# Kernel optimization log

Hardware: AMD Instinct MI355X
Metric: run time of the kernel (lower is better)

Reference implementation:

```python
import jax, jax.numpy as jnp
import numpy as np

B, D, H, NL, DFF, N = 64, 768, 12, 12, 3072, 197
HD = D // H  # 64
SCALE = HD ** -0.5


def setup_inputs() -> dict:
    key = jax.random.key(0)
    ks = iter(jax.random.split(key, 64))
    def rn(shape, s=0.02):
        return jax.random.normal(next(ks), shape, jnp.float32) * s
    inp = {
        'x': jax.random.normal(next(ks), (B, 12, 1000), jnp.float32),
        # PatchEmbed convs (torch Conv1d weight layout OIH)
        'conv1_w': rn((256, 12, 5), 0.1), 'conv1_b': jnp.zeros((256,), jnp.float32),
        'bn1_g': jnp.ones((256,), jnp.float32), 'bn1_b': jnp.zeros((256,), jnp.float32),
        'bn1_m': jnp.zeros((256,), jnp.float32), 'bn1_v': jnp.ones((256,), jnp.float32),
        'conv2_w': rn((768, 256, 5), 0.05), 'conv2_b': jnp.zeros((768,), jnp.float32),
        'bn2_g': jnp.ones((768,), jnp.float32), 'bn2_b': jnp.zeros((768,), jnp.float32),
        'bn2_m': jnp.zeros((768,), jnp.float32), 'bn2_v': jnp.ones((768,), jnp.float32),
        'cls_token': rn((1, 1, D)), 'pos_embed': rn((1, N, D)),
        # 12 transformer blocks, stacked. Linear weights stored [in, out].
        'ln1_g': jnp.ones((NL, D), jnp.float32), 'ln1_b': jnp.zeros((NL, D), jnp.float32),
        'qkv_w': rn((NL, D, 3 * D)),            # qkv_bias=False
        'proj_w': rn((NL, D, D)), 'proj_b': jnp.zeros((NL, D), jnp.float32),
        'ln2_g': jnp.ones((NL, D), jnp.float32), 'ln2_b': jnp.zeros((NL, D), jnp.float32),
        'fc1_w': rn((NL, D, DFF)), 'fc1_b': jnp.zeros((NL, DFF), jnp.float32),
        'fc2_w': rn((NL, DFF, D)), 'fc2_b': jnp.zeros((NL, D), jnp.float32),
        'norm_g': jnp.ones((D,), jnp.float32), 'norm_b': jnp.zeros((D,), jnp.float32),
        # ProjectionHead (nonlinear): Linear(768->768,no bias)+BN, ReLU, Linear(768->512,no bias)+BN
        'p1_w': rn((D, D)),
        'p1bn_g': jnp.ones((D,), jnp.float32), 'p1bn_b': jnp.zeros((D,), jnp.float32),
        'p1bn_m': jnp.zeros((D,), jnp.float32), 'p1bn_v': jnp.ones((D,), jnp.float32),
        'p2_w': rn((D, 512)),
        'p2bn_g': jnp.ones((512,), jnp.float32), 'p2bn_b': jnp.zeros((512,), jnp.float32),
        'p2bn_m': jnp.zeros((512,), jnp.float32), 'p2bn_v': jnp.ones((512,), jnp.float32),
    }
    return inp


def _conv1d(x, w, b, stride):
    y = jax.lax.conv_general_dilated(x, w, (stride,), 'VALID',
                                     dimension_numbers=('NCH', 'OIH', 'NCH'))
    return y + b[None, :, None]


def _bn_c(x, g, b, m, v, eps=1e-5):  # BatchNorm1d eval, channel axis 1 of (B,C,L)
    return (x - m[None, :, None]) * (g[None, :, None] / jnp.sqrt(v[None, :, None] + eps)) + b[None, :, None]


def _bn_f(x, g, b, m, v, eps=1e-5):  # BatchNorm1d eval on (B,F)
    return (x - m) * (g / jnp.sqrt(v + eps)) + b


def _ln(x, g, b, eps=1e-6):
    mu = x.mean(-1, keepdims=True)
    var = jnp.var(x, axis=-1, keepdims=True)
    return (x - mu) * jax.lax.rsqrt(var + eps) * g + b


def reference(x, conv1_w, conv1_b, bn1_g, bn1_b, bn1_m, bn1_v,
              conv2_w, conv2_b, bn2_g, bn2_b, bn2_m, bn2_v,
              cls_token, pos_embed,
              ln1_g, ln1_b, qkv_w, proj_w, proj_b,
              ln2_g, ln2_b, fc1_w, fc1_b, fc2_w, fc2_b,
              norm_g, norm_b,
              p1_w, p1bn_g, p1bn_b, p1bn_m, p1bn_v,
              p2_w, p2bn_g, p2bn_b, p2bn_m, p2bn_v):
    # PatchEmbed: conv -> ReLU -> BN, twice; then (B, 196, 768)
    h = _bn_c(jax.nn.relu(_conv1d(x, conv1_w, conv1_b, 5)), bn1_g, bn1_b, bn1_m, bn1_v)
    h = _bn_c(jax.nn.relu(_conv1d(h, conv2_w, conv2_b, 1)), bn2_g, bn2_b, bn2_m, bn2_v)
    h = jnp.transpose(h, (0, 2, 1))  # [B, 196, D]
    b = h.shape[0]
    tok = jnp.concatenate([jnp.broadcast_to(cls_token, (b, 1, D)), h], axis=1) + pos_embed  # [B, 197, D]

    for i in range(NL):
        y = _ln(tok, ln1_g[i], ln1_b[i])
        qkv = jnp.einsum('bnd,de->bne', y, qkv_w[i]).reshape(b, N, 3, H, HD)
        q, k, v = jnp.moveaxis(qkv, 2, 0)  # each [B, N, H, HD]
        q = jnp.transpose(q, (0, 2, 1, 3)) * SCALE  # [B, H, N, HD]
        k = jnp.transpose(k, (0, 2, 1, 3))
        v = jnp.transpose(v, (0, 2, 1, 3))
        attn = jax.nn.softmax(jnp.einsum('bhnd,bhmd->bhnm', q, k), axis=-1)
        o = jnp.einsum('bhnm,bhmd->bhnd', attn, v)
        o = jnp.transpose(o, (0, 2, 1, 3)).reshape(b, N, D)
        tok = tok + jnp.einsum('bnd,de->bne', o, proj_w[i]) + proj_b[i]
        y = _ln(tok, ln2_g[i], ln2_b[i])
        y = jax.nn.gelu(jnp.einsum('bnd,df->bnf', y, fc1_w[i]) + fc1_b[i], approximate=False)
        tok = tok + jnp.einsum('bnf,fd->bnd', y, fc2_w[i]) + fc2_b[i]

    cls = _ln(tok, norm_g, norm_b)[:, 0]  # global_pool='token'
    z = _bn_f(cls @ p1_w, p1bn_g, p1bn_b, p1bn_m, p1bn_v)
    z = jax.nn.relu(z)
    z = _bn_f(z @ p2_w, p2bn_g, p2bn_b, p2bn_m, p2bn_v)
    return z
```

## Files before the change

kernel.cpp:

```cpp
#include <hip/hip_runtime.h>
#include <hip/hip_bf16.h>

typedef __hip_bfloat16 bf16;
typedef __attribute__((ext_vector_type(8))) short bf16x8;
typedef __attribute__((ext_vector_type(4))) float f32x4;

__device__ __forceinline__ float bf2f(bf16 v) { return __bfloat162float(v); }
__device__ __forceinline__ unsigned short f2bfu(float f) {
    bf16 h = __float2bfloat16(f);
    return __builtin_bit_cast(unsigned short, h);
}

__device__ __forceinline__ void gload16(const void* g, void* lds) {
    __builtin_amdgcn_global_load_lds(
        (const __attribute__((address_space(1))) unsigned int*)g,
        (__attribute__((address_space(3))) unsigned int*)lds, 16, 0, 0);
}

__global__ __launch_bounds__(256)
void conv1_kernel(const float* __restrict__ x, const float* __restrict__ w,
                  const float* __restrict__ bias,
                  const float* __restrict__ g, const float* __restrict__ b,
                  const float* __restrict__ m, const float* __restrict__ v,
                  bf16* __restrict__ h1) {
    int bo = blockIdx.x;
    int bb = bo >> 8, o = bo & 255;
    int l = threadIdx.x;
    if (l >= 200) return;
    const float* wo = w + o * 60;
    const float* xb = x + bb * 12000;
    float acc = bias[o];
#pragma unroll
    for (int i = 0; i < 12; i++)
#pragma unroll
        for (int t = 0; t < 5; t++)
            acc = fmaf(xb[i * 1000 + 5 * l + t], wo[i * 5 + t], acc);
    acc = fmaxf(acc, 0.f);
    float sc = g[o] * rsqrtf(v[o] + 1e-5f);
    acc = (acc - m[o]) * sc + b[o];
    h1[bo * 200 + l] = __float2bfloat16(acc);
}

__global__ __launch_bounds__(256)
void im2col_kernel(const bf16* __restrict__ h1, bf16* __restrict__ A2) {
    int idx = blockIdx.x * 256 + threadIdx.x;
    int row = idx / 1280, c = idx - row * 1280;
    int bb = row / 196, l = row - bb * 196;
    int i = c / 5, t = c - i * 5;
    A2[idx] = h1[(bb * 256 + i) * 200 + l + t];
}

__global__ __launch_bounds__(256)
void add_cls_pos(const float* __restrict__ cls, const float* __restrict__ pos,
                 float* __restrict__ tok) {
    int idx = blockIdx.x * 256 + threadIdx.x;
    int bb = idx / 768, d = idx - bb * 768;
    tok[(size_t)bb * 197 * 768 + d] = cls[d] + pos[d];
}

__global__ __launch_bounds__(256)
void cvt_kernel(const float* __restrict__ in, bf16* __restrict__ out, int n) {
    int idx = blockIdx.x * 256 + threadIdx.x;
    if (idx < n) out[idx] = __float2bfloat16(in[idx]);
}

__global__ __launch_bounds__(256)
void wtrans_layer(const float* __restrict__ qkvw, const float* __restrict__ projw,
                  const float* __restrict__ fc1w, const float* __restrict__ fc2w,
                  bf16* __restrict__ qkvT, bf16* __restrict__ projT,
                  bf16* __restrict__ fc1T, bf16* __restrict__ fc2T) {
    __shared__ float tile[32][33];
    int blk = blockIdx.x;
    const float* in; bf16* out; int Kd, Nd, t0;
    if (blk < 1728)      { in = qkvw; out = qkvT; Kd = 768;  Nd = 2304; t0 = blk; }
    else if (blk < 2304) { in = projw; out = projT; Kd = 768;  Nd = 768;  t0 = blk - 1728; }
    else if (blk < 4608) { in = fc1w; out = fc1T; Kd = 768;  Nd = 3072; t0 = blk - 2304; }
    else                 { in = fc2w; out = fc2T; Kd = 3072; Nd = 768;  t0 = blk - 4608; }
    int ntiles = Nd >> 5;
    int kt = t0 / ntiles, nt = t0 - kt * ntiles;
    int k0 = kt * 32, n0 = nt * 32;
    int tx = threadIdx.x & 31, ty = threadIdx.x >> 5;
#pragma unroll
    for (int j = 0; j < 4; j++)
        tile[ty + 8 * j][tx] = in[(size_t)(k0 + ty + 8 * j) * Nd + n0 + tx];
    __syncthreads();
#pragma unroll
    for (int j = 0; j < 4; j++)
        out[(size_t)(n0 + ty + 8 * j) * Kd + k0 + tx] = __float2bfloat16(tile[tx][ty + 8 * j]);
}

__global__ __launch_bounds__(256)
void wtrans2(const float* __restrict__ in, bf16* __restrict__ out, int Kd, int Nd) {
    __shared__ float tile[32][33];
    int ntiles = Nd >> 5;
    int kt = blockIdx.x / ntiles, nt = blockIdx.x - kt * ntiles;
    int k0 = kt * 32, n0 = nt * 32;
    int tx = threadIdx.x & 31, ty = threadIdx.x >> 5;
#pragma unroll
    for (int j = 0; j < 4; j++)
        tile[ty + 8 * j][tx] = in[(size_t)(k0 + ty + 8 * j) * Nd + n0 + tx];
    __syncthreads();
#pragma unroll
    for (int j = 0; j < 4; j++)
        out[(size_t)(n0 + ty + 8 * j) * Kd + k0 + tx] = __float2bfloat16(tile[tx][ty + 8 * j]);
}

__global__ __launch_bounds__(256)
void ln_kernel(const float* __restrict__ x, bf16* __restrict__ y,
               const float* __restrict__ g, const float* __restrict__ b,
               int nrows, int xstride) {
    int row = blockIdx.x * 4 + (threadIdx.x >> 6);
    if (row >= nrows) return;
    int l = threadIdx.x & 63;
    const float* xr = x + (size_t)row * xstride;
    float4 v0 = *(const float4*)(xr + l * 4);
    float4 v1 = *(const float4*)(xr + 256 + l * 4);
    float4 v2 = *(const float4*)(xr + 512 + l * 4);
    float s1 = 0.f, s2 = 0.f;
    {
        float e;
        e = v0.x; s1 += e; s2 += e * e;  e = v0.y; s1 += e; s2 += e * e;
        e = v0.z; s1 += e; s2 += e * e;  e = v0.w; s1 += e; s2 += e * e;
        e = v1.x; s1 += e; s2 += e * e;  e = v1.y; s1 += e; s2 += e * e;
        e = v1.z; s1 += e; s2 += e * e;  e = v1.w; s1 += e; s2 += e * e;
        e = v2.x; s1 += e; s2 += e * e;  e = v2.y; s1 += e; s2 += e * e;
        e = v2.z; s1 += e; s2 += e * e;  e = v2.w; s1 += e; s2 += e * e;
    }
#pragma unroll
    for (int off = 1; off < 64; off <<= 1) {
        s1 += __shfl_xor(s1, off);
        s2 += __shfl_xor(s2, off);
    }
    float mu = s1 * (1.f / 768.f);
    float rs = rsqrtf(s2 * (1.f / 768.f) - mu * mu + 1e-6f);
    bf16* yr = y + (size_t)row * 768;
#pragma unroll
    for (int sgi = 0; sgi < 3; sgi++) {
        float4 vv = sgi == 0 ? v0 : (sgi == 1 ? v1 : v2);
        float4 gg = *(const float4*)(g + sgi * 256 + l * 4);
        float4 bb = *(const float4*)(b + sgi * 256 + l * 4);
        ushort4 o;
        o.x = f2bfu((vv.x - mu) * rs * gg.x + bb.x);
        o.y = f2bfu((vv.y - mu) * rs * gg.y + bb.y);
        o.z = f2bfu((vv.z - mu) * rs * gg.z + bb.z);
        o.w = f2bfu((vv.w - mu) * rs * gg.w + bb.w);
        *(ushort4*)(yr + sgi * 256 + l * 4) = o;
    }
}

enum { E_BF16 = 0, E_RESID = 1, E_GELU = 2, E_CONV2 = 3, E_HEAD1 = 4, E_HEAD2 = 5 };

template<int EPI>
__global__ __launch_bounds__(256)
void gemm2(const bf16* __restrict__ A, const bf16* __restrict__ Bt,
           int M, int N, int K,
           const float* __restrict__ bias,
           bf16* __restrict__ Co, float* __restrict__ tok,
           const float* __restrict__ bng, const float* __restrict__ bnb,
           const float* __restrict__ bnm, const float* __restrict__ bnv,
           const float* __restrict__ pos) {
    __shared__ bf16 As[128 * 64];
    __shared__ bf16 Bs[128 * 64];
    const int t = threadIdx.x;
    const int l = t & 63, w = t >> 6;
    const int wm = (w >> 1) * 64, wn = (w & 1) * 64;
    const int row0 = blockIdx.y * 128, col0 = blockIdx.x * 128;
    const int lr = l & 15, kg = l >> 4;

    const int srow = w * 8 + (l >> 3);
    const int sc = ((l & 7) ^ (l >> 3)) * 8;
    const int dstoff = w * 1024 + l * 16;

    const f32x4 zero4 = {0.f, 0.f, 0.f, 0.f};
    f32x4 acc[4][4];
#pragma unroll
    for (int i = 0; i < 4; i++)
#pragma unroll
        for (int j = 0; j < 4; j++) acc[i][j] = zero4;

    for (int k0 = 0; k0 < K; k0 += 64) {
#pragma unroll
        for (int p = 0; p < 4; p++) {
            int r = srow + p * 32;
            int gra = row0 + r; if (gra >= M) gra = M - 1;
            gload16(A + (size_t)gra * K + k0 + sc, (char*)As + p * 4096 + dstoff);
            gload16(Bt + (size_t)(col0 + r) * K + k0 + sc, (char*)Bs + p * 4096 + dstoff);
        }
        __syncthreads();
#pragma unroll
        for (int ks = 0; ks < 2; ks++) {
            bf16x8 af[4], bfv[4];
            const int cc = ((ks * 4 + kg) ^ (lr & 7)) * 16;
#pragma unroll
            for (int i = 0; i < 4; i++) {
                af[i]  = *(const bf16x8*)((const char*)As + (wm + i * 16 + lr) * 128 + cc);
                bfv[i] = *(const bf16x8*)((const char*)Bs + (wn + i * 16 + lr) * 128 + cc);
            }
#pragma unroll
            for (int i = 0; i < 4; i++)
#pragma unroll
                for (int j = 0; j < 4; j++)
                    acc[i][j] = __builtin_amdgcn_mfma_f32_16x16x32_bf16(af[i], bfv[j], acc[i][j], 0, 0, 0);
        }
        __syncthreads();
    }

    const int rbase = row0 + wm + (kg << 2);
#pragma unroll
    for (int i = 0; i < 4; i++) {
#pragma unroll
        for (int sr = 0; sr < 4; sr++) {
            int r = rbase + i * 16 + sr;
            if (r < M) {
#pragma unroll
                for (int j = 0; j < 4; j++) {
                    int c = col0 + wn + j * 16 + lr;
                    float vv = acc[i][j][sr];
                    if (EPI == E_BF16) {
                        Co[(size_t)r * N + c] = __float2bfloat16(vv);
                    } else if (EPI == E_RESID) {
                        float* p = tok + (size_t)r * N + c;
                        *p += vv + bias[c];
                    } else if (EPI == E_GELU) {
                        float xx = vv + bias[c];
                        float gg = 0.5f * xx * (1.f + erff(xx * 0.70710678118f));
                        Co[(size_t)r * N + c] = __float2bfloat16(gg);
                    } else if (EPI == E_CONV2) {
                        float xx = vv + bias[c];
                        xx = fmaxf(xx, 0.f);
                        float sc2 = bng[c] * rsqrtf(bnv[c] + 1e-5f);
                        xx = (xx - bnm[c]) * sc2 + bnb[c];
                        int bb = r / 196, ll = r - bb * 196;
                        xx += pos[(size_t)(1 + ll) * 768 + c];
                        tok[(size_t)(bb * 197 + 1 + ll) * 768 + c] = xx;
                    } else if (EPI == E_HEAD1) {
                        float sc2 = bng[c] * rsqrtf(bnv[c] + 1e-5f);
                        float xx = (vv - bnm[c]) * sc2 + bnb[c];
                        xx = fmaxf(xx, 0.f);
                        Co[(size_t)r * N + c] = __float2bfloat16(xx);
                    } else {
                        float sc2 = bng[c] * rsqrtf(bnv[c] + 1e-5f);
                        tok[(size_t)r * N + c] = (vv - bnm[c]) * sc2 + bnb[c];
                    }
                }
            }
        }
    }
}

#define ATTN_LDS (208 * 72 * 2 + 64 * 232 * 2 + 4 * 16 * 232 * 2)

__global__ __launch_bounds__(256)
void attn_kernel(const bf16* __restrict__ qkv, bf16* __restrict__ o) {
    extern __shared__ char smem[];
    bf16* Ks = (bf16*)smem;
    bf16* Vt = Ks + 208 * 72;
    bf16* Pl = Vt + 64 * 232;
    const int bh = blockIdx.x, bb = bh / 12, h = bh - bb * 12;
    const int t = threadIdx.x, w = t >> 6, l = t & 63;
    const int lr = l & 15, lk8 = (l >> 4) * 8;
    const size_t base = (size_t)bb * 197 * 2304 + (size_t)h * 64;

    for (int qi = t; qi < 197 * 16; qi += 256) {
        int n = qi >> 4, d4 = (qi & 15) << 2;
        ushort4 kv = *(const ushort4*)(qkv + base + (size_t)n * 2304 + 768 + d4);
        *(ushort4*)&Ks[n * 72 + d4] = kv;
    }
    for (int qi = t; qi < 11 * 72; qi += 256) ((unsigned short*)Ks)[197 * 72 + qi] = 0;
    for (int qi = t; qi < 197 * 16; qi += 256) {
        int n = qi >> 4, d4 = (qi & 15) << 2;
        ushort4 vv = *(const ushort4*)(qkv + base + (size_t)n * 2304 + 1536 + d4);
        ((unsigned short*)Vt)[(d4 + 0) * 232 + n] = vv.x;
        ((unsigned short*)Vt)[(d4 + 1) * 232 + n] = vv.y;
        ((unsigned short*)Vt)[(d4 + 2) * 232 + n] = vv.z;
        ((unsigned short*)Vt)[(d4 + 3) * 232 + n] = vv.w;
    }
    for (int qi = t; qi < 64 * 35; qi += 256) {
        int d = qi / 35, c = 197 + (qi - d * 35);
        ((unsigned short*)Vt)[d * 232 + c] = 0;
    }
    __syncthreads();

    bf16* Pw = Pl + w * (16 * 232);
    const f32x4 zero4 = {0.f, 0.f, 0.f, 0.f};
    for (int qt = w; qt < 13; qt += 4) {
        int m0 = qt * 16;
        int qrow = m0 + lr; if (qrow > 196) qrow = 196;
        const bf16* qp = qkv + (size_t)(bb * 197 + qrow) * 2304 + h * 64 + lk8;
        bf16x8 a0 = *(const bf16x8*)qp;
        bf16x8 a1 = *(const bf16x8*)(qp + 32);
        f32x4 s[13];
#pragma unroll
        for (int kt = 0; kt < 13; kt++) {
            const bf16* kp = &Ks[(kt * 16 + lr) * 72 + lk8];
            bf16x8 b0 = *(const bf16x8*)kp;
            bf16x8 b1 = *(const bf16x8*)(kp + 32);
            f32x4 z = zero4;
            z = __builtin_amdgcn_mfma_f32_16x16x32_bf16(a0, b0, z, 0, 0, 0);
            z = __builtin_amdgcn_mfma_f32_16x16x32_bf16(a1, b1, z, 0, 0, 0);
            s[kt] = z;
        }
        float mx[4] = {-1e30f, -1e30f, -1e30f, -1e30f};
#pragma unroll
        for (int kt = 0; kt < 13; kt++) {
            bool valid = (kt < 12) || (lr <= 4);
#pragma unroll
            for (int sr = 0; sr < 4; sr++) {
                float sv = s[kt][sr] * 0.125f;
                sv = valid ? sv : -1e30f;
                s[kt][sr] = sv;
                mx[sr] = fmaxf(mx[sr], sv);
            }
        }
#pragma unroll
        for (int off = 1; off < 16; off <<= 1)
#pragma unroll
            for (int sr = 0; sr < 4; sr++)
                mx[sr] = fmaxf(mx[sr], __shfl_xor(mx[sr], off));
        float sum[4] = {0.f, 0.f, 0.f, 0.f};
#pragma unroll
        for (int kt = 0; kt < 13; kt++)
#pragma unroll
            for (int sr = 0; sr < 4; sr++) {
                float p = __expf(s[kt][sr] - mx[sr]);
                s[kt][sr] = p;
                sum[sr] += p;
            }
#pragma unroll
        for (int off = 1; off < 16; off <<= 1)
#pragma unroll
            for (int sr = 0; sr < 4; sr++)
                sum[sr] += __shfl_xor(sum[sr], off);
        float inv[4];
#pragma unroll
        for (int sr = 0; sr < 4; sr++) inv[sr] = 1.f / sum[sr];
#pragma unroll
        for (int kt = 0; kt < 13; kt++)
#pragma unroll
            for (int sr = 0; sr < 4; sr++)
                ((unsigned short*)Pw)[((l >> 4) * 4 + sr) * 232 + kt * 16 + lr] =
                    f2bfu(s[kt][sr] * inv[sr]);
        for (int j = l; j < 256; j += 64) {
            int rr = j >> 4, cc = 208 + (j & 15);
            ((unsigned short*)Pw)[rr * 232 + cc] = 0;
        }
        asm volatile("s_waitcnt lgkmcnt(0)" ::: "memory");
        f32x4 oa[4];
#pragma unroll
        for (int nf = 0; nf < 4; nf++) oa[nf] = zero4;
#pragma unroll
        for (int ks = 0; ks < 7; ks++) {
            const bf16* pp = &Pw[lr * 232 + ks * 32 + lk8];
            bf16x8 ap = *(const bf16x8*)pp;
#pragma unroll
            for (int nf = 0; nf < 4; nf++) {
                bf16x8 bv = *(const bf16x8*)&Vt[(nf * 16 + lr) * 232 + ks * 32 + lk8];
                oa[nf] = __builtin_amdgcn_mfma_f32_16x16x32_bf16(ap, bv, oa[nf], 0, 0, 0);
            }
        }
#pragma unroll
        for (int nf = 0; nf < 4; nf++)
#pragma unroll
            for (int sr = 0; sr < 4; sr++) {
                int orow = m0 + (l >> 4) * 4 + sr;
                if (orow <= 196)
                    o[(size_t)(bb * 197 + orow) * 768 + h * 64 + nf * 16 + lr] =
                        __float2bfloat16(oa[nf][sr]);
            }
    }
}

extern "C" void kernel_launch(void* const* d_in, const int* in_sizes, int n_in,
                              void* d_out, int out_size, void* d_ws, size_t ws_size,
                              hipStream_t stream) {
    (void)in_sizes; (void)n_in; (void)out_size; (void)ws_size;
    const float* x        = (const float*)d_in[0];
    const float* conv1_w  = (const float*)d_in[1];
    const float* conv1_b  = (const float*)d_in[2];
    const float* bn1_g = (const float*)d_in[3],  *bn1_b = (const float*)d_in[4];
    const float* bn1_m = (const float*)d_in[5],  *bn1_v = (const float*)d_in[6];
    const float* conv2_w  = (const float*)d_in[7];
    const float* conv2_b  = (const float*)d_in[8];
    const float* bn2_g = (const float*)d_in[9],  *bn2_b = (const float*)d_in[10];
    const float* bn2_m = (const float*)d_in[11], *bn2_v = (const float*)d_in[12];
    const float* cls_tok  = (const float*)d_in[13];
    const float* pos      = (const float*)d_in[14];
    const float* ln1_g = (const float*)d_in[15], *ln1_b = (const float*)d_in[16];
    const float* qkv_w = (const float*)d_in[17];
    const float* proj_w = (const float*)d_in[18], *proj_b = (const float*)d_in[19];
    const float* ln2_g = (const float*)d_in[20], *ln2_b = (const float*)d_in[21];
    const float* fc1_w = (const float*)d_in[22], *fc1_b = (const float*)d_in[23];
    const float* fc2_w = (const float*)d_in[24], *fc2_b = (const float*)d_in[25];
    const float* norm_g = (const float*)d_in[26], *norm_b = (const float*)d_in[27];
    const float* p1_w = (const float*)d_in[28];
    const float* p1g = (const float*)d_in[29], *p1b = (const float*)d_in[30];
    const float* p1m = (const float*)d_in[31], *p1v = (const float*)d_in[32];
    const float* p2_w = (const float*)d_in[33];
    const float* p2g = (const float*)d_in[34], *p2b = (const float*)d_in[35];
    const float* p2m = (const float*)d_in[36], *p2v = (const float*)d_in[37];

    char* ws = (char*)d_ws;
    float* tok  = (float*)(ws + 0);
    bf16* ybf   = (bf16*)(ws + 38731776);
    bf16* qkvb  = (bf16*)(ws + 58097664);
    bf16* a1    = (bf16*)(ws + 116195328);
    bf16* h1    = (bf16*)(ws + 116195328);
    bf16* A2    = (bf16*)(ws + 116195328 + 8388608);
    bf16* clsb  = (bf16*)(ws + 193658880);
    bf16* z1    = (bf16*)(ws + 193757184);
    bf16* wtb   = (bf16*)(ws + 193953792);
    bf16* qkvT = wtb;
    bf16* projT = wtb + 1769472;
    bf16* fc1T = wtb + 2359296;
    bf16* fc2T = wtb + 4718592;
    bf16* conv2T = wtb;
    bf16* p1T = a1;
    bf16* p2T = a1 + 768 * 768;

    (void)hipFuncSetAttribute((const void*)attn_kernel,
                              hipFuncAttributeMaxDynamicSharedMemorySize, ATTN_LDS);

    conv1_kernel<<<64 * 256, 256, 0, stream>>>(x, conv1_w, conv1_b, bn1_g, bn1_b, bn1_m, bn1_v, h1);
    im2col_kernel<<<(12544 * 1280) / 256, 256, 0, stream>>>(h1, A2);
    cvt_kernel<<<(768 * 1280 + 255) / 256, 256, 0, stream>>>(conv2_w, conv2T, 768 * 1280);
    gemm2<E_CONV2><<<dim3(6, 98), 256, 0, stream>>>(
        A2, conv2T, 12544, 768, 1280, conv2_b, nullptr, tok, bn2_g, bn2_b, bn2_m, bn2_v, pos);
    add_cls_pos<<<(64 * 768) / 256, 256, 0, stream>>>(cls_tok, pos, tok);

    const int MT = (12608 + 127) / 128;
    for (int i = 0; i < 12; i++) {
        wtrans_layer<<<6912, 256, 0, stream>>>(
            qkv_w + (size_t)i * 768 * 2304, proj_w + (size_t)i * 768 * 768,
            fc1_w + (size_t)i * 768 * 3072, fc2_w + (size_t)i * 3072 * 768,
            qkvT, projT, fc1T, fc2T);
        ln_kernel<<<12608 / 4, 256, 0, stream>>>(tok, ybf, ln1_g + i * 768, ln1_b + i * 768, 12608, 768);
        gemm2<E_BF16><<<dim3(18, MT), 256, 0, stream>>>(
            ybf, qkvT, 12608, 2304, 768,
            nullptr, qkvb, nullptr, nullptr, nullptr, nullptr, nullptr, nullptr);
        attn_kernel<<<768, 256, ATTN_LDS, stream>>>(qkvb, ybf);
        gemm2<E_RESID><<<dim3(6, MT), 256, 0, stream>>>(
            ybf, projT, 12608, 768, 768,
            proj_b + i * 768, nullptr, tok, nullptr, nullptr, nullptr, nullptr, nullptr);
        ln_kernel<<<12608 / 4, 256, 0, stream>>>(tok, ybf, ln2_g + i * 768, ln2_b + i * 768, 12608, 768);
        gemm2<E_GELU><<<dim3(24, MT), 256, 0, stream>>>(
            ybf, fc1T, 12608, 3072, 768,
            fc1_b + i * 3072, a1, nullptr, nullptr, nullptr, nullptr, nullptr, nullptr);
        gemm2<E_RESID><<<dim3(6, MT), 256, 0, stream>>>(
            a1, fc2T, 12608, 768, 3072,
            fc2_b + i * 768, nullptr, tok, nullptr, nullptr, nullptr, nullptr, nullptr);
    }

    ln_kernel<<<16, 256, 0, stream>>>(tok, clsb, norm_g, norm_b, 64, 197 * 768);
    wtrans2<<<576, 256, 0, stream>>>(p1_w, p1T, 768, 768);
    wtrans2<<<384, 256, 0, stream>>>(p2_w, p2T, 768, 512);
    gemm2<E_HEAD1><<<dim3(6, 1), 256, 0, stream>>>(
        clsb, p1T, 64, 768, 768,
        nullptr, z1, nullptr, p1g, p1b, p1m, p1v, nullptr);
    gemm2<E_HEAD2><<<dim3(4, 1), 256, 0, stream>>>(
        z1, p2T, 64, 512, 768,
        nullptr, nullptr, (float*)d_out, p2g, p2b, p2m, p2v, nullptr);
}
```

Before: 4.988 ms.

## Double-buffer GEMM LDS tiles and switch GELU to tanh approximation

The bf16 MFMA GEMM now uses 64 KB of dynamic shared memory holding two tile buffers. The global-to-LDS loads for the next K tile are issued before computing on the current one, so memory latency overlaps the matrix math, with a single barrier per iteration. The larger LDS footprint may lower how many blocks fit on a CU. Separately, the exact erf GELU in the fc1 epilogue is replaced by a tanh approximation built on __expf. That is cheaper but departs slightly from the reference's approximate=False semantics.

```diff
diff --git a/kernel.cpp b/kernel.cpp
--- a/kernel.cpp
+++ b/kernel.cpp
@@ -15,6 +15,14 @@
     __builtin_amdgcn_global_load_lds(
         (const __attribute__((address_space(1))) unsigned int*)g,
         (__attribute__((address_space(3))) unsigned int*)lds, 16, 0, 0);
+}
+
+__device__ __forceinline__ float gelu_f(float x) {
+    float u = 0.7978845608f * (x + 0.044715f * x * x * x);
+    float e = __expf(-2.0f * fabsf(u));
+    float th = (1.f - e) / (1.f + e);
+    th = u < 0.f ? -th : th;
+    return 0.5f * x * (1.f + th);
 }
 
 __global__ __launch_bounds__(256)
@@ -149,6 +157,7 @@
 }
 
 enum { E_BF16 = 0, E_RESID = 1, E_GELU = 2, E_CONV2 = 3, E_HEAD1 = 4, E_HEAD2 = 5 };
+#define GEMM_LDS 65536
 
 template<int EPI>
 __global__ __launch_bounds__(256)
@@ -159,8 +168,7 @@
            const float* __restrict__ bng, const float* __restrict__ bnb,
            const float* __restrict__ bnm, const float* __restrict__ bnv,
            const float* __restrict__ pos) {
-    __shared__ bf16 As[128 * 64];
-    __shared__ bf16 Bs[128 * 64];
+    extern __shared__ char smem[];
     const int t = threadIdx.x;
     const int l = t & 63, w = t >> 6;
     const int wm = (w >> 1) * 64, wn = (w & 1) * 64;
@@ -178,23 +186,35 @@
 #pragma unroll
         for (int j = 0; j < 4; j++) acc[i][j] = zero4;
 
-    for (int k0 = 0; k0 < K; k0 += 64) {
+    auto stage = [&](int b, int k0) {
 #pragma unroll
         for (int p = 0; p < 4; p++) {
             int r = srow + p * 32;
             int gra = row0 + r; if (gra >= M) gra = M - 1;
-            gload16(A + (size_t)gra * K + k0 + sc, (char*)As + p * 4096 + dstoff);
-            gload16(Bt + (size_t)(col0 + r) * K + k0 + sc, (char*)Bs + p * 4096 + dstoff);
-        }
-        __syncthreads();
+            char* base = smem + b * 32768 + p * 4096 + dstoff;
+            gload16(A + (size_t)gra * K + k0 + sc, base);
+            gload16(Bt + (size_t)(col0 + r) * K + k0 + sc, base + 16384);
+        }
+    };
+
+    const int nt = K >> 6;
+    stage(0, 0);
+    asm volatile("s_waitcnt vmcnt(0)" ::: "memory");
+    __syncthreads();
+
+    int cur = 0;
+    for (int kt = 0; kt < nt; kt++) {
+        if (kt + 1 < nt) stage(cur ^ 1, (kt + 1) << 6);
+        const char* Ab = smem + cur * 32768;
+        const char* Bb = Ab + 16384;
 #pragma unroll
         for (int ks = 0; ks < 2; ks++) {
             bf16x8 af[4], bfv[4];
             const int cc = ((ks * 4 + kg) ^ (lr & 7)) * 16;
 #pragma unroll
             for (int i = 0; i < 4; i++) {
-                af[i]  = *(const bf16x8*)((const char*)As + (wm + i * 16 + lr) * 128 + cc);
-                bfv[i] = *(const bf16x8*)((const char*)Bs + (wn + i * 16 + lr) * 128 + cc);
+                af[i]  = *(const bf16x8*)(Ab + (wm + i * 16 + lr) * 128 + cc);
+                bfv[i] = *(const bf16x8*)(Bb + (wn + i * 16 + lr) * 128 + cc);
             }
 #pragma unroll
             for (int i = 0; i < 4; i++)
@@ -202,7 +222,9 @@
                 for (int j = 0; j < 4; j++)
                     acc[i][j] = __builtin_amdgcn_mfma_f32_16x16x32_bf16(af[i], bfv[j], acc[i][j], 0, 0, 0);
         }
+        asm volatile("s_waitcnt vmcnt(0)" ::: "memory");
         __syncthreads();
+        cur ^= 1;
     }
 
     const int rbase = row0 + wm + (kg << 2);
@@ -222,9 +244,7 @@
                         float* p = tok + (size_t)r * N + c;
                         *p += vv + bias[c];
                     } else if (EPI == E_GELU) {
-                        float xx = vv + bias[c];
-                        float gg = 0.5f * xx * (1.f + erff(xx * 0.70710678118f));
-                        Co[(size_t)r * N + c] = __float2bfloat16(gg);
+                        Co[(size_t)r * N + c] = __float2bfloat16(gelu_f(vv + bias[c]));
                     } else if (EPI == E_CONV2) {
                         float xx = vv + bias[c];
                         xx = fmaxf(xx, 0.f);
@@ -419,11 +439,23 @@
 
     (void)hipFuncSetAttribute((const void*)attn_kernel,
                               hipFuncAttributeMaxDynamicSharedMemorySize, ATTN_LDS);
+    (void)hipFuncSetAttribute((const void*)gemm2<E_BF16>,
+                              hipFuncAttributeMaxDynamicSharedMemorySize, GEMM_LDS);
+    (void)hipFuncSetAttribute((const void*)gemm2<E_RESID>,
+                              hipFuncAttributeMaxDynamicSharedMemorySize, GEMM_LDS);
+    (void)hipFuncSetAttribute((const void*)gemm2<E_GELU>,
+                              hipFuncAttributeMaxDynamicSharedMemorySize, GEMM_LDS);
+    (void)hipFuncSetAttribute((const void*)gemm2<E_CONV2>,
+                              hipFuncAttributeMaxDynamicSharedMemorySize, GEMM_LDS);
+    (void)hipFuncSetAttribute((const void*)gemm2<E_HEAD1>,
+                              hipFuncAttributeMaxDynamicSharedMemorySize, GEMM_LDS);
+    (void)hipFuncSetAttribute((const void*)gemm2<E_HEAD2>,
+                              hipFuncAttributeMaxDynamicSharedMemorySize, GEMM_LDS);
 
     conv1_kernel<<<64 * 256, 256, 0, stream>>>(x, conv1_w, conv1_b, bn1_g, bn1_b, bn1_m, bn1_v, h1);
     im2col_kernel<<<(12544 * 1280) / 256, 256, 0, stream>>>(h1, A2);
     cvt_kernel<<<(768 * 1280 + 255) / 256, 256, 0, stream>>>(conv2_w, conv2T, 768 * 1280);
-    gemm2<E_CONV2><<<dim3(6, 98), 256, 0, stream>>>(
+    gemm2<E_CONV2><<<dim3(6, 98), 256, GEMM_LDS, stream>>>(
         A2, conv2T, 12544, 768, 1280, conv2_b, nullptr, tok, bn2_g, bn2_b, bn2_m, bn2_v, pos);
     add_cls_pos<<<(64 * 768) / 256, 256, 0, stream>>>(cls_tok, pos, tok);
 
@@ -434,18 +466,18 @@
             fc1_w + (size_t)i * 768 * 3072, fc2_w + (size_t)i * 3072 * 768,
             qkvT, projT, fc1T, fc2T);
         ln_kernel<<<12608 / 4, 256, 0, stream>>>(tok, ybf, ln1_g + i * 768, ln1_b + i * 768, 12608, 768);
-        gemm2<E_BF16><<<dim3(18, MT), 256, 0, stream>>>(
+        gemm2<E_BF16><<<dim3(18, MT), 256, GEMM_LDS, stream>>>(
             ybf, qkvT, 12608, 2304, 768,
             nullptr, qkvb, nullptr, nullptr, nullptr, nullptr, nullptr, nullptr);
         attn_kernel<<<768, 256, ATTN_LDS, stream>>>(qkvb, ybf);
-        gemm2<E_RESID><<<dim3(6, MT), 256, 0, stream>>>(
+        gemm2<E_RESID><<<dim3(6, MT), 256, GEMM_LDS, stream>>>(
             ybf, projT, 12608, 768, 768,
             proj_b + i * 768, nullptr, tok, nullptr, nullptr, nullptr, nullptr, nullptr);
         ln_kernel<<<12608 / 4, 256, 0, stream>>>(tok, ybf, ln2_g + i * 768, ln2_b + i * 768, 12608, 768);
-        gemm2<E_GELU><<<dim3(24, MT), 256, 0, stream>>>(
+        gemm2<E_GELU><<<dim3(24, MT), 256, GEMM_LDS, stream>>>(
             ybf, fc1T, 12608, 3072, 768,
             fc1_b + i * 3072, a1, nullptr, nullptr, nullptr, nullptr, nullptr, nullptr);
-        gemm2<E_RESID><<<dim3(6, MT), 256, 0, stream>>>(
+        gemm2<E_RESID><<<dim3(6, MT), 256, GEMM_LDS, stream>>>(
             a1, fc2T, 12608, 768, 3072,
             fc2_b + i * 768, nullptr, tok, nullptr, nullptr, nullptr, nullptr, nullptr);
     }
@@ -453,10 +485,10 @@
     ln_kernel<<<16, 256, 0, stream>>>(tok, clsb, norm_g, norm_b, 64, 197 * 768);
     wtrans2<<<576, 256, 0, stream>>>(p1_w, p1T, 768, 768);
     wtrans2<<<384, 256, 0, stream>>>(p2_w, p2T, 768, 512);
-    gemm2<E_HEAD1><<<dim3(6, 1), 256, 0, stream>>>(
+    gemm2<E_HEAD1><<<dim3(6, 1), 256, GEMM_LDS, stream>>>(
         clsb, p1T, 64, 768, 768,
         nullptr, z1, nullptr, p1g, p1b, p1m, p1v, nullptr);
-    gemm2<E_HEAD2><<<dim3(4, 1), 256, 0, stream>>>(
+    gemm2<E_HEAD2><<<dim3(4, 1), 256, GEMM_LDS, stream>>>(
         z1, p2T, 64, 512, 768,
         nullptr, nullptr, (float*)d_out, p2g, p2b, p2m, p2v, nullptr);
 }
```

After: 5.083 ms. Within noise of the previous version (+1.9%).
